# Optimization experiments

Measured on AMD Instinct MI355X. Metric: run time of the kernel, lower is better.

The kernel has to match this reference:

```python
import jax, jax.numpy as jnp
import numpy as np

SELF_DIM = 36
ENT_DIM = 28
HID = 256


def setup_inputs() -> dict:
    key = jax.random.key(0)
    ks = jax.random.split(key, 12)
    B, agent_num, n_noisy = 32768, 20, 20
    obs_dim = SELF_DIM + ENT_DIM * (2 * agent_num - 1 + n_noisy)
    s = 0.02
    return {
        "x": jax.random.normal(ks[0], (B, obs_dim), dtype=jnp.float32),
        "Watt": jax.random.normal(ks[1], (ENT_DIM + SELF_DIM, 1), jnp.float32) * s,
        "batt": jnp.zeros((1,), jnp.float32),
        "We": jax.random.normal(ks[2], (ENT_DIM + SELF_DIM, HID), jnp.float32) * s,
        "be": jnp.zeros((HID,), jnp.float32),
        "Wse": jax.random.normal(ks[3], (2 * SELF_DIM, HID), jnp.float32) * s,
        "bse": jnp.zeros((HID,), jnp.float32),
        "Wg": jax.random.normal(ks[4], (3 * HID, 3), jnp.float32) * s,
        "bg": jnp.zeros((3,), jnp.float32),
        "Wo": jax.random.normal(ks[5], (2 * HID, HID), jnp.float32) * s,
        "bo": jnp.zeros((HID,), jnp.float32),
        "agent_num": agent_num,
    }


def reference(x, Watt, batt, We, be, Wse, bse, Wg, bg, Wo, bo, agent_num):
    B = x.shape[0]
    self_info = x[:, :SELF_DIM]  # [B,36]
    opp_end = SELF_DIM + ENT_DIM * agent_num
    par_end = opp_end + ENT_DIM * (agent_num - 1)
    opps = x[:, SELF_DIM:opp_end].reshape(B, agent_num, ENT_DIM)
    pars = x[:, opp_end:par_end].reshape(B, agent_num - 1, ENT_DIM)
    noisy = x[:, par_end:].reshape(B, -1, ENT_DIM)

    def pool(ent):
        # additive-attention pooling over one entity group
        n = ent.shape[1]
        os_ = jnp.concatenate(
            [jnp.broadcast_to(self_info[:, None, :], (B, n, SELF_DIM)), ent], axis=2
        )  # [B,n,64]
        att = jax.nn.softmax(os_ @ Watt + batt, axis=1)  # [B,n,1]
        es = os_ @ We + be  # [B,n,H]
        return jnp.sum(att * es, axis=1)  # [B,H]

    opp_e, par_e, noi_e = pool(opps), pool(pars), pool(noisy)
    group_e = jnp.stack([opp_e, par_e, noi_e], axis=1)  # [B,3,H]
    gw = jax.nn.softmax(
        jnp.concatenate([opp_e, par_e, noi_e], axis=1) @ Wg + bg, axis=1
    )  # [B,3]
    other = jnp.einsum("bg,bgh->bh", gw, group_e)  # [B,H]
    self_e = jnp.concatenate([self_info, self_info], axis=1) @ Wse + bse  # [B,H]
    obs_embedding = jnp.concatenate([other, self_e], axis=1)  # [B,2H]
    return obs_embedding @ Wo + bo
```

## Files before the change

### kernel.cpp

```cpp
#include <hip/hip_runtime.h>
#include <hip/hip_bf16.h>

#define SELF_D 36
#define ENT_D  28
#define HID    256
#define OBS    1688
#define NWAVES 8192

#define WS_A     0
#define WS_B     9216
#define WS_C     16384
#define WS_MSEL  16640
#define WS_MENT  16748
#define WS_CG    17000
#define WS_WATT  17008
#define WS_AT    17040
#define WS_BT    26256
#define WS_TOTAL 33424

__global__ __launch_bounds__(256)
void setup_kernel(const float* __restrict__ Watt, const float* __restrict__ We,
                  const float* __restrict__ be,  const float* __restrict__ Wse,
                  const float* __restrict__ bse, const float* __restrict__ Wg,
                  const float* __restrict__ bg,  const float* __restrict__ Wo,
                  const float* __restrict__ bo,  float* __restrict__ ws) {
  const int blk = blockIdx.x;
  const int c = threadIdx.x;
  if (blk < 36) {
    int k = blk;
    float acc = 0.f;
    for (int r = 0; r < 256; ++r) acc += We[k*256 + r] * Wo[r*256 + c];
    for (int r = 0; r < 256; ++r) acc += (Wse[k*256 + r] + Wse[(36+k)*256 + r]) * Wo[(256+r)*256 + c];
    ws[WS_A + k*256 + c] = acc;
    ws[WS_AT + c*36 + k] = acc;
  } else if (blk < 64) {
    int k = blk - 36;
    float acc = 0.f;
    for (int r = 0; r < 256; ++r) acc += We[(36+k)*256 + r] * Wo[r*256 + c];
    ws[WS_B + k*256 + c] = acc;
    ws[WS_BT + c*28 + k] = acc;
  } else if (blk == 64) {
    float acc = bo[c];
    for (int r = 0; r < 256; ++r) acc += be[r] * Wo[r*256 + c];
    for (int r = 0; r < 256; ++r) acc += bse[r] * Wo[(256+r)*256 + c];
    ws[WS_C + c] = acc;
  } else {
    for (int t = c; t < 391; t += 256) {
      if (t < 108) {
        int k = t / 3, j = t - 3*k;
        float acc = 0.f;
        for (int r = 0; r < 256; ++r) {
          float wg = Wg[r*3 + j] + Wg[(256+r)*3 + j] + Wg[(512+r)*3 + j];
          acc += We[k*256 + r] * wg;
        }
        ws[WS_MSEL + t] = acc;
      } else if (t < 360) {
        int idx = t - 108;
        int g = idx / 84, rem = idx - 84*g;
        int k = rem / 3, j = rem - 3*k;
        float acc = 0.f;
        for (int r = 0; r < 256; ++r) acc += We[(36+k)*256 + r] * Wg[(256*g + r)*3 + j];
        ws[WS_MENT + idx] = acc;
      } else if (t < 363) {
        int j = t - 360;
        float acc = bg[j];
        for (int r = 0; r < 256; ++r)
          acc += be[r] * (Wg[r*3 + j] + Wg[(256+r)*3 + j] + Wg[(512+r)*3 + j]);
        ws[WS_CG + j] = acc;
      } else {
        int k = t - 363;
        ws[WS_WATT + k] = Watt[36 + k];
      }
    }
  }
}

__device__ __forceinline__ unsigned pack_bf2(float a, float b) {
  unsigned ua = __float_as_uint(a);
  unsigned ub = __float_as_uint(b);
  ua = (ua + 0x7fffu + ((ua >> 16) & 1u)) >> 16;
  ub = (ub + 0x7fffu + ((ub >> 16) & 1u)) & 0xffff0000u;
  return ua | ub;
}
__device__ __forceinline__ float bf_lo(unsigned u) { return __uint_as_float(u << 16); }
__device__ __forceinline__ float bf_hi(unsigned u) { return __uint_as_float(u & 0xffff0000u); }
__device__ __forceinline__ float bperm(int idx4, float v) {
  return __int_as_float(__builtin_amdgcn_ds_bpermute(idx4, __float_as_int(v)));
}

__global__ __launch_bounds__(256)
void pool_kernel(const float* __restrict__ x, const float* __restrict__ ws,
                 float* __restrict__ out, int B) {
  __shared__ __align__(16) unsigned short tileh[4][60*28];
  __shared__ __align__(16) float sself[4][40];
  __shared__ __align__(16) float sebar[4][88];

  const int tid = threadIdx.x;
  const int w = tid >> 6, ln = tid & 63;

  if (ln < 7) ((uint2*)&tileh[w][39*28])[ln] = make_uint2(0u, 0u);

  const float* Wp = ws + WS_WATT;
  const float cg0 = ws[WS_CG + 0], cg1 = ws[WS_CG + 1], cg2 = ws[WS_CG + 2];

  int  soff[7]; bool went[7];
#pragma unroll
  for (int i = 0; i < 7; ++i) {
    int q = i*64 + ln;
    bool v = (q >= 9) && (q < 422);
    went[i] = v;
    int qm = v ? (q - 9) : 0;
    int e = qm / 7, t = qm - 7*e;
    int s = e + (e >= 39 ? 1 : 0);
    soff[i] = s*28 + 4*t;
  }
  const bool wself = (ln < 9);

  const bool lval = (ln < 60) && (ln != 39);
  const int  lrow = (ln < 60 ? ln : 0) * 28;

  int rotb[5];
  {
    int base = (ln < 60) ? (ln/20)*20 : 60;
    int n    = (ln < 60) ? 20 : 4;
    int off  = ln - base;
    const int rs[5] = {1, 2, 4, 8, 16};
#pragma unroll
    for (int j = 0; j < 5; ++j) rotb[j] = (base + (off + rs[j]) % n) * 4;
  }

  const bool mact = (ln < 21);
  const int  mg = ln / 7, mkq = ln - 7*mg;
  const int  mrow0 = (mg*20)*28 + 4*mkq;

  const int  gj = ln >> 4, gch = ln & 15;
  const bool gact = (gj < 3) && (gch < 15);
  float gw8[8];
#pragma unroll
  for (int q = 0; q < 8; ++q)
    gw8[q] = gact ? ws[WS_MSEL + (q*15 + gch)*3 + gj] : 0.f;

  const int row0 = blockIdx.x * 4 + w;

  float4 pf[7];
  if (row0 < B) {
    const float4* xr = (const float4*)(x + (size_t)row0 * OBS);
#pragma unroll
    for (int i = 0; i < 7; ++i) { int idx = i*64 + ln; if (idx < 422) pf[i] = xr[idx]; }
  }

  for (int row = row0; row < B; row += NWAVES) {
    if (wself) *(float4*)&sself[w][ln*4] = pf[0];
#pragma unroll
    for (int i = 0; i < 7; ++i) {
      if (went[i]) {
        uint2 u = make_uint2(pack_bf2(pf[i].x, pf[i].y), pack_bf2(pf[i].z, pf[i].w));
        *(uint2*)&tileh[w][soff[i]] = u;
      }
    }

    {
      int nr = row + NWAVES;
      if (nr < B) {
        const float4* xn = (const float4*)(x + (size_t)nr * OBS);
#pragma unroll
        for (int i = 0; i < 7; ++i) { int idx = i*64 + ln; if (idx < 422) pf[i] = xn[idx]; }
      }
    }
    asm volatile("" ::: "memory");

    float4 ev[7];
    float l = -1e30f;
    {
      float acc = 0.f;
#pragma unroll
      for (int t = 0; t < 7; ++t) {
        uint2 u = *(const uint2*)&tileh[w][lrow + 4*t];
        ev[t].x = bf_lo(u.x); ev[t].y = bf_hi(u.x);
        ev[t].z = bf_lo(u.y); ev[t].w = bf_hi(u.y);
        acc += ev[t].x*Wp[4*t] + ev[t].y*Wp[4*t+1] + ev[t].z*Wp[4*t+2] + ev[t].w*Wp[4*t+3];
      }
      if (lval) l = acc;
    }

    float m = l;
#pragma unroll
    for (int off = 32; off; off >>= 1) m = fmaxf(m, __shfl_xor(m, off));
    float a = lval ? __expf(l - m) : 0.f;
    float w2  = a  + bperm(rotb[0], a);
    float w4  = w2 + bperm(rotb[1], w2);
    float w8  = w4 + bperm(rotb[2], w4);
    float w16 = w8 + bperm(rotb[3], w8);
    float us  = w16 + bperm(rotb[4], w4);
    float an  = a / us;

    if (ln < 60) {
#pragma unroll
      for (int t = 0; t < 7; ++t) {
        uint2 u = make_uint2(pack_bf2(ev[t].x*an, ev[t].y*an),
                             pack_bf2(ev[t].z*an, ev[t].w*an));
        *(uint2*)&tileh[w][lrow + 4*t] = u;
      }
    }
    asm volatile("" ::: "memory");

    if (mact) {
      float s0 = 0.f, s1 = 0.f, s2 = 0.f, s3 = 0.f;
#pragma unroll
      for (int i = 0; i < 20; ++i) {
        uint2 u = *(const uint2*)&tileh[w][mrow0 + i*28];
        s0 += bf_lo(u.x); s1 += bf_hi(u.x);
        s2 += bf_lo(u.y); s3 += bf_hi(u.y);
      }
      *(float4*)&sebar[w][mg*28 + 4*mkq] = make_float4(s0, s1, s2, s3);
    }
    asm volatile("" ::: "memory");

    float gl = 0.f;
    if (gact) {
#pragma unroll
      for (int q = 0; q < 8; ++q) {
        int c = q*15 + gch;
        float v = (c < SELF_D) ? sself[w][c] : sebar[w][c - SELF_D];
        gl += v * gw8[q];
      }
    }
#pragma unroll
    for (int off = 1; off < 16; off <<= 1) gl += __shfl_xor(gl, off);
    float l0 = __shfl(gl, 0)  + cg0;
    float l1 = __shfl(gl, 16) + cg1;
    float l2 = __shfl(gl, 32) + cg2;
    float mm = fmaxf(l0, fmaxf(l1, l2));
    float e0x = __expf(l0 - mm), e1x = __expf(l1 - mm), e2x = __expf(l2 - mm);
    float inv = 1.f / (e0x + e1x + e2x);

    float fv;
    if (ln < SELF_D) {
      fv = sself[w][ln];
    } else {
      int k = ln - SELF_D;
      fv = (e0x * sebar[w][k] + e1x * sebar[w][28 + k] + e2x * sebar[w][56 + k]) * inv;
    }
    out[(size_t)row * HID + ln] = fv;
  }
}

#define PR_ROWS 32
#define PR_CH   8
__global__ __launch_bounds__(256)
void proj_kernel(const float* __restrict__ ws, float* __restrict__ out) {
  __shared__ __align__(16) float sf[PR_CH][64];
  const int tid = threadIdx.x;

  float4 Av[9], Bv[7];
#pragma unroll
  for (int q = 0; q < 9; ++q) Av[q] = ((const float4*)(ws + WS_AT + tid * 36))[q];
#pragma unroll
  for (int q = 0; q < 7; ++q) Bv[q] = ((const float4*)(ws + WS_BT + tid * 28))[q];
  const float cc = ws[WS_C + tid];

  const size_t row0 = (size_t)blockIdx.x * PR_ROWS;
  for (int chk = 0; chk < PR_ROWS / PR_CH; ++chk) {
    const size_t rbase = row0 + chk * PR_CH;
    if (tid < PR_CH * 16) {
      int r = tid >> 4, q = tid & 15;
      ((float4*)&sf[r][0])[q] = ((const float4*)(out + (rbase + r) * HID))[q];
    }
    __syncthreads();
#pragma unroll
    for (int r = 0; r < PR_CH; ++r) {
      float acc = cc;
      const float4* f4 = (const float4*)&sf[r][0];
#pragma unroll
      for (int q = 0; q < 9; ++q) {
        float4 s = f4[q];
        acc += Av[q].x*s.x + Av[q].y*s.y + Av[q].z*s.z + Av[q].w*s.w;
      }
#pragma unroll
      for (int q = 0; q < 7; ++q) {
        float4 s = f4[9 + q];
        acc += Bv[q].x*s.x + Bv[q].y*s.y + Bv[q].z*s.z + Bv[q].w*s.w;
      }
      out[(rbase + r) * HID + tid] = acc;
    }
    __syncthreads();
  }
}

extern "C" void kernel_launch(void* const* d_in, const int* in_sizes, int n_in,
                              void* d_out, int out_size, void* d_ws, size_t ws_size,
                              hipStream_t stream) {
  const float* x    = (const float*)d_in[0];
  const float* Watt = (const float*)d_in[1];
  const float* We   = (const float*)d_in[3];
  const float* be   = (const float*)d_in[4];
  const float* Wse  = (const float*)d_in[5];
  const float* bse  = (const float*)d_in[6];
  const float* Wg   = (const float*)d_in[7];
  const float* bg   = (const float*)d_in[8];
  const float* Wo   = (const float*)d_in[9];
  const float* bo   = (const float*)d_in[10];
  float* out = (float*)d_out;
  float* ws  = (float*)d_ws;
  const int B = in_sizes[0] / OBS;

  setup_kernel<<<66, 256, 0, stream>>>(Watt, We, be, Wse, bse, Wg, bg, Wo, bo, ws);
  pool_kernel<<<NWAVES / 4, 256, 0, stream>>>(x, ws, out, B);
  proj_kernel<<<B / PR_ROWS, 256, 0, stream>>>(ws, out);
}
```

Measured before the change: 112.2 us.

## Fuse pooling and output projection into one persistent kernel

Merges the pooling kernel and the projection kernel so each block pools four rows into shared memory and immediately applies the 64-to-256 projection, writing final outputs. This removes the intermediate 64-float feature write and re-read through the output buffer and one kernel launch. In exchange it adds per-iteration block barriers and many more live registers (the projection weights), with launch bounds removed, which may cut occupancy for the memory-bound pooling stage.

```diff
diff --git a/kernel.cpp b/kernel.cpp
--- a/kernel.cpp
+++ b/kernel.cpp
@@ -5,7 +5,7 @@
 #define ENT_D  28
 #define HID    256
 #define OBS    1688
-#define NWAVES 8192
+#define GRID   2048
 
 #define WS_A     0
 #define WS_B     9216
@@ -88,12 +88,12 @@
   return __int_as_float(__builtin_amdgcn_ds_bpermute(idx4, __float_as_int(v)));
 }
 
-__global__ __launch_bounds__(256)
-void pool_kernel(const float* __restrict__ x, const float* __restrict__ ws,
-                 float* __restrict__ out, int B) {
+__global__ void fused_kernel(const float* __restrict__ x, const float* __restrict__ ws,
+                             float* __restrict__ out, int B) {
   __shared__ __align__(16) unsigned short tileh[4][60*28];
   __shared__ __align__(16) float sself[4][40];
   __shared__ __align__(16) float sebar[4][88];
+  __shared__ __align__(16) float sf[4][64];
 
   const int tid = threadIdx.x;
   const int w = tid >> 6, ln = tid & 63;
@@ -102,6 +102,13 @@
 
   const float* Wp = ws + WS_WATT;
   const float cg0 = ws[WS_CG + 0], cg1 = ws[WS_CG + 1], cg2 = ws[WS_CG + 2];
+
+  float4 Av[9], Bv[7];
+#pragma unroll
+  for (int q = 0; q < 9; ++q) Av[q] = ((const float4*)(ws + WS_AT + tid * 36))[q];
+#pragma unroll
+  for (int q = 0; q < 7; ++q) Bv[q] = ((const float4*)(ws + WS_BT + tid * 28))[q];
+  const float cc = ws[WS_C + tid];
 
   int  soff[7]; bool went[7];
 #pragma unroll
@@ -140,16 +147,19 @@
   for (int q = 0; q < 8; ++q)
     gw8[q] = gact ? ws[WS_MSEL + (q*15 + gch)*3 + gj] : 0.f;
 
-  const int row0 = blockIdx.x * 4 + w;
+  const int ngrp = B / 4;
 
   float4 pf[7];
-  if (row0 < B) {
-    const float4* xr = (const float4*)(x + (size_t)row0 * OBS);
-#pragma unroll
-    for (int i = 0; i < 7; ++i) { int idx = i*64 + ln; if (idx < 422) pf[i] = xr[idx]; }
-  }
-
-  for (int row = row0; row < B; row += NWAVES) {
+  {
+    int row = blockIdx.x * 4 + w;
+    if (row < B) {
+      const float4* xr = (const float4*)(x + (size_t)row * OBS);
+#pragma unroll
+      for (int i = 0; i < 7; ++i) { int idx = i*64 + ln; if (idx < 422) pf[i] = xr[idx]; }
+    }
+  }
+
+  for (int grp = blockIdx.x; grp < ngrp; grp += GRID) {
     if (wself) *(float4*)&sself[w][ln*4] = pf[0];
 #pragma unroll
     for (int i = 0; i < 7; ++i) {
@@ -160,7 +170,7 @@
     }
 
     {
-      int nr = row + NWAVES;
+      int nr = (grp + GRID) * 4 + w;
       if (nr < B) {
         const float4* xn = (const float4*)(x + (size_t)nr * OBS);
 #pragma unroll
@@ -241,47 +251,27 @@
       int k = ln - SELF_D;
       fv = (e0x * sebar[w][k] + e1x * sebar[w][28 + k] + e2x * sebar[w][56 + k]) * inv;
     }
-    out[(size_t)row * HID + ln] = fv;
-  }
-}
-
-#define PR_ROWS 32
-#define PR_CH   8
-__global__ __launch_bounds__(256)
-void proj_kernel(const float* __restrict__ ws, float* __restrict__ out) {
-  __shared__ __align__(16) float sf[PR_CH][64];
-  const int tid = threadIdx.x;
-
-  float4 Av[9], Bv[7];
-#pragma unroll
-  for (int q = 0; q < 9; ++q) Av[q] = ((const float4*)(ws + WS_AT + tid * 36))[q];
-#pragma unroll
-  for (int q = 0; q < 7; ++q) Bv[q] = ((const float4*)(ws + WS_BT + tid * 28))[q];
-  const float cc = ws[WS_C + tid];
-
-  const size_t row0 = (size_t)blockIdx.x * PR_ROWS;
-  for (int chk = 0; chk < PR_ROWS / PR_CH; ++chk) {
-    const size_t rbase = row0 + chk * PR_CH;
-    if (tid < PR_CH * 16) {
-      int r = tid >> 4, q = tid & 15;
-      ((float4*)&sf[r][0])[q] = ((const float4*)(out + (rbase + r) * HID))[q];
-    }
+    sf[w][ln] = fv;
     __syncthreads();
-#pragma unroll
-    for (int r = 0; r < PR_CH; ++r) {
-      float acc = cc;
-      const float4* f4 = (const float4*)&sf[r][0];
-#pragma unroll
-      for (int q = 0; q < 9; ++q) {
-        float4 s = f4[q];
-        acc += Av[q].x*s.x + Av[q].y*s.y + Av[q].z*s.z + Av[q].w*s.w;
-      }
-#pragma unroll
-      for (int q = 0; q < 7; ++q) {
-        float4 s = f4[9 + q];
-        acc += Bv[q].x*s.x + Bv[q].y*s.y + Bv[q].z*s.z + Bv[q].w*s.w;
-      }
-      out[(rbase + r) * HID + tid] = acc;
+
+    {
+      float* o = out + (size_t)grp * (4 * HID) + tid;
+#pragma unroll
+      for (int r = 0; r < 4; ++r) {
+        float acc = cc;
+        const float4* f4 = (const float4*)&sf[r][0];
+#pragma unroll
+        for (int q = 0; q < 9; ++q) {
+          float4 s = f4[q];
+          acc += Av[q].x*s.x + Av[q].y*s.y + Av[q].z*s.z + Av[q].w*s.w;
+        }
+#pragma unroll
+        for (int q = 0; q < 7; ++q) {
+          float4 s = f4[9 + q];
+          acc += Bv[q].x*s.x + Bv[q].y*s.y + Bv[q].z*s.z + Bv[q].w*s.w;
+        }
+        o[(size_t)r * HID] = acc;
+      }
     }
     __syncthreads();
   }
@@ -305,6 +295,5 @@
   const int B = in_sizes[0] / OBS;
 
   setup_kernel<<<66, 256, 0, stream>>>(Watt, We, be, Wse, bse, Wg, bg, Wo, bo, ws);
-  pool_kernel<<<NWAVES / 4, 256, 0, stream>>>(x, ws, out, B);
-  proj_kernel<<<B / PR_ROWS, 256, 0, stream>>>(ws, out);
-}
+  fused_kernel<<<GRID, 256, 0, stream>>>(x, ws, out, B);
+}
```

After: 243.0 us. 2.17x slower.
